# Performance work log

Measured on AMD Instinct MI355X. Metric: run time of the kernel, lower is better.

Reference implementation:

```python
import jax, jax.numpy as jnp
import numpy as np
import math

TILE_SIZE = 32
N_HEADS = 16
FACTOR = 5.0
MASK_VALUE = -1e9


def setup_inputs() -> dict:
    key = jax.random.key(0)
    ks = jax.random.split(key, 8)
    B, S, D = 2, 2048, 1024
    w = 0.02  # weight scale so attention logits stay in a sane range
    return {
        "query": jax.random.normal(ks[0], (B, S, D), jnp.float32),
        "key": jax.random.normal(ks[1], (B, S, D), jnp.float32),
        "value": jax.random.normal(ks[2], (B, S, D), jnp.float32),
        "mask": jnp.zeros((1, 1, S, S), jnp.float32),
        "Wq": jax.random.normal(ks[3], (D, D), jnp.float32) * w,
        "bq": jnp.zeros((D,), jnp.float32),
        "Wk": jax.random.normal(ks[4], (D, D), jnp.float32) * w,
        "bk": jnp.zeros((D,), jnp.float32),
        "Wv": jax.random.normal(ks[5], (D, D), jnp.float32) * w,
        "bv": jnp.zeros((D,), jnp.float32),
        "Wo": jax.random.normal(ks[6], (D, D), jnp.float32) * w,
        "bo": jnp.zeros((D,), jnp.float32),
        "q_valid_len": 2000,
        "k_valid_len": 1900,
    }


def _pad_to_multiple(x, multiple):
    L = x.shape[1]
    p = (-L) % multiple  # static
    if p:
        x = jnp.pad(x, ((0, 0), (0, p), (0, 0)))
    return x, L


def _split_heads(x, H):
    B, L, D = x.shape
    return x.reshape(B, L, H, D // H).transpose(0, 2, 1, 3)  # [B,H,L,hd]


def _forward(query, key, value, mask, Wq, bq, Wk, bk, Wv, bv, Wo, bo,
             q_valid_len, k_valid_len):
    B, Sq, D = query.shape
    H = N_HEADS
    hd = D // H
    q = query @ Wq.T + bq
    k = key @ Wk.T + bk
    v = value @ Wv.T + bv
    q, q_len_pad = _pad_to_multiple(q, TILE_SIZE)
    k, _ = _pad_to_multiple(k, TILE_SIZE)
    v, _ = _pad_to_multiple(v, TILE_SIZE)
    qh, kh, vh = _split_heads(q, H), _split_heads(k, H), _split_heads(v, H)
    Lq, Lk = qh.shape[2], kh.shape[2]

    # key padding mask [1,1,1,Lk]
    kpm = ((jnp.arange(Lk) >= k_valid_len).astype(jnp.float32) * MASK_VALUE)
    attn_mask = mask + kpm.reshape(1, 1, 1, Lk)

    # manual scaled-dot attention with bf16 cast of scores (stable softmax path)
    scores = jnp.einsum('bhqd,bhkd->bhqk', qh, kh) / math.sqrt(hd)
    scores = scores.astype(jnp.bfloat16) + attn_mask.astype(jnp.bfloat16)
    probs = jax.nn.softmax(scores, axis=-1).astype(vh.dtype)
    context = jnp.einsum('bhqk,bhkd->bhqd', probs, vh)

    # ProbSparse top-u query-selection mask (note: original passes q_len_pad,
    # the pre-padding length, as valid_length)
    u = max(1, int(FACTOR * math.log(max(2, q_valid_len))))
    q_norm = jnp.sum(qh * qh, axis=-1)  # [B,H,Lq]
    if q_len_pad < Lq:
        q_norm = jnp.where(jnp.arange(Lq) < q_len_pad, q_norm, MASK_VALUE)
    _, topk_idx = jax.lax.top_k(q_norm, u)  # [B,H,u]
    # scatter ones at top-u positions (indices unique -> one-hot sum == set)
    ps_mask = jnp.sum(jax.nn.one_hot(topk_idx, Lq, dtype=jnp.float32), axis=2)
    context = context * ps_mask[..., None]

    # merge heads, strip padding, output projection (dropout p=0 / eval)
    context = context.transpose(0, 2, 1, 3).reshape(B, Lq, D)[:, :Sq, :]
    return context @ Wo.T + bo


def reference(query, key, value, mask, Wq, bq, Wk, bk, Wv, bv, Wo, bo,
              q_valid_len, k_valid_len):
    return _forward(query, key, value, mask, Wq, bq, Wk, bk, Wv, bv, Wo, bo,
                    q_valid_len, k_valid_len)
```

## Files before the change

kernel.cpp:

```cpp
#include <hip/hip_runtime.h>

typedef unsigned short u16;
typedef __bf16 bf16x8 __attribute__((ext_vector_type(8)));
typedef float f32x4 __attribute__((ext_vector_type(4)));

__device__ __forceinline__ u16 f2bf(float f){
  unsigned int x = __float_as_uint(f);
  unsigned int r = (x + 0x7FFFu + ((x >> 16) & 1u)) >> 16;
  return (u16)r;
}
__device__ __forceinline__ float bf2f(u16 u){
  return __uint_as_float(((unsigned int)u) << 16);
}
__device__ __forceinline__ int compute_u(int qvlv){
  int mm = qvlv > 2 ? qvlv : 2;
  int u = (int)(5.0 * log((double)mm));
  if (u < 1) u = 1;
  if (u > 64) u = 64;
  return u;
}
__device__ __forceinline__ void gload_lds16(const void* g, void* l){
  __builtin_amdgcn_global_load_lds(
      (const __attribute__((address_space(1))) void*)g,
      (__attribute__((address_space(3))) void*)l, 16, 0, 0);
}

__global__ void expand_kernel(const float* __restrict__ xq, const float* __restrict__ xk,
                              const float* __restrict__ xv,
                              const float* __restrict__ wq, const float* __restrict__ wk,
                              const float* __restrict__ wv,
                              u16* __restrict__ X1, u16* __restrict__ X2,
                              u16* __restrict__ W1, u16* __restrict__ W2,
                              const float* __restrict__ Wo, float* __restrict__ WoT,
                              unsigned int* __restrict__ hmask)
{
  __shared__ float tile[32][33];
  int t = threadIdx.x;
  if (blockIdx.x >= 7680){
    int bid = blockIdx.x - 7680;
    int bx = (bid & 31) * 32, by = (bid >> 5) * 32;
    int tx = t & 31, ty = t >> 5;
#pragma unroll
    for (int r = 0; r < 4; ++r)
      tile[ty + r*8][tx] = Wo[(size_t)(by + ty + r*8) * 1024 + bx + tx];
    __syncthreads();
#pragma unroll
    for (int r = 0; r < 4; ++r)
      WoT[(size_t)(bx + ty + r*8) * 1024 + by + tx] = tile[tx][ty + r*8];
    return;
  }
  size_t g = (size_t)blockIdx.x * 256 + t;
  if (g < 4096) hmask[g] = 0;
  const float* src; u16 *d1, *d2;
  if (g < 1572864ull) {
    int p = (int)(g >> 19);
    size_t e = (g & 524287ull) * 8;
    src = (p == 0 ? xq : (p == 1 ? xk : xv)) + e;
    size_t o = (size_t)p * 4194304ull + e;
    d1 = X1 + o; d2 = X2 + o;
  } else {
    size_t wg = g - 1572864ull;
    int p = (int)(wg >> 17);
    size_t e = (wg & 131071ull) * 8;
    src = (p == 0 ? wq : (p == 1 ? wk : wv)) + e;
    size_t o = (size_t)p * 1048576ull + e;
    d1 = W1 + o; d2 = W2 + o;
  }
  float4 a = *reinterpret_cast<const float4*>(src);
  float4 b = *reinterpret_cast<const float4*>(src + 4);
  float xs[8] = {a.x, a.y, a.z, a.w, b.x, b.y, b.z, b.w};
  unsigned int hw[4], lw[4];
#pragma unroll
  for (int i = 0; i < 4; ++i){
    u16 h0 = f2bf(xs[2*i]);     u16 l0 = f2bf(xs[2*i]     - bf2f(h0));
    u16 h1 = f2bf(xs[2*i + 1]); u16 l1 = f2bf(xs[2*i + 1] - bf2f(h1));
    hw[i] = (unsigned int)h0 | ((unsigned int)h1 << 16);
    lw[i] = (unsigned int)l0 | ((unsigned int)l1 << 16);
  }
  *reinterpret_cast<uint4*>(d1) = make_uint4(hw[0], hw[1], hw[2], hw[3]);
  *reinterpret_cast<uint4*>(d2) = make_uint4(lw[0], lw[1], lw[2], lw[3]);
}

__global__ __launch_bounds__(512, 1) void gemm_proj(
    const u16* __restrict__ X1, const u16* __restrict__ X2,
    const u16* __restrict__ W1, const u16* __restrict__ W2,
    const float* __restrict__ bq, const float* __restrict__ bk, const float* __restrict__ bv,
    float* __restrict__ PROJ, float* __restrict__ qn)
{
  int z = blockIdx.z;
  int orig = blockIdx.x + blockIdx.y * 8;
  int wgid = (orig & 7) * 16 + (orig >> 3);
  int bx = wgid & 7, by = wgid >> 3;

  const u16* Xa0 = X1 + (size_t)z * 4194304;
  const u16* Xa1 = X2 + (size_t)z * 4194304;
  const u16* Wb0 = W1 + (size_t)z * 1048576;
  const u16* Wb1 = W2 + (size_t)z * 1048576;
  const float* bias = (z == 0) ? bq : (z == 1 ? bk : bv);
  float* C = PROJ + (size_t)z * 4194304;

  __shared__ __align__(16) u16 T[2 * 24576];
  u16* SET0 = T;
  u16* SET1 = T + 24576;

  int t = threadIdx.x;
  int wave = t >> 6, lane = t & 63;
  int wm = wave >> 1, wn = wave & 1;
  int lr = lane & 15, lk = lane >> 4;
  int rowA = by * 256, rowB = bx * 128;
  f32x4 acc[4][4] = {};
  bf16x8 afA[4], afB[4], bgA[4], bgB[4];

#define STAGEA(dstbase, G)                                                    \
  {                                                                           \
    _Pragma("unroll")                                                         \
    for (int i = 0; i < 2; ++i){                                              \
      int p = i * 512 + t;                                                    \
      int r = p >> 2;                                                         \
      int c = (p & 3) ^ ((r >> 1) & 3);                                       \
      gload_lds16(G + (size_t)(rowA + r) * 1024 + pk + c * 8,                 \
                  (dstbase) + p * 8);                                         \
    }                                                                         \
  }
#define STAGEB(dstbase, G)                                                    \
  {                                                                           \
    int p = t;                                                                \
    int r = p >> 2;                                                           \
    int c = (p & 3) ^ ((r >> 1) & 3);                                         \
    gload_lds16(G + (size_t)(rowB + r) * 1024 + pk + c * 8,                   \
                (dstbase) + p * 8);                                           \
  }
#define STAGE_SET(S)                                                          \
  {                                                                           \
    STAGEA((S), Xa0); STAGEA((S) + 8192, Xa1);                                \
    STAGEB((S) + 16384, Wb0); STAGEB((S) + 20480, Wb1);                       \
  }
#define LOADA(dst, tile)                                                      \
  {                                                                           \
    _Pragma("unroll")                                                         \
    for (int m = 0; m < 4; ++m){                                              \
      int r = wm * 64 + m * 16 + lr;                                          \
      dst[m] = *reinterpret_cast<const bf16x8*>(                              \
          &(tile)[r * 32 + ((lk ^ ((r >> 1) & 3)) << 3)]);                    \
    }                                                                         \
  }
#define LOADB(dst, tile)                                                      \
  {                                                                           \
    _Pragma("unroll")                                                         \
    for (int n = 0; n < 4; ++n){                                              \
      int r = wn * 64 + n * 16 + lr;                                          \
      dst[n] = *reinterpret_cast<const bf16x8*>(                              \
          &(tile)[r * 32 + ((lk ^ ((r >> 1) & 3)) << 3)]);                    \
    }                                                                         \
  }
#define GRPX(A_, B_)                                                          \
  {                                                                           \
    __builtin_amdgcn_s_setprio(1);                                            \
    _Pragma("unroll")                                                         \
    for (int m = 0; m < 4; ++m)                                               \
      _Pragma("unroll")                                                       \
      for (int n = 0; n < 4; ++n)                                             \
        acc[m][n] = __builtin_amdgcn_mfma_f32_16x16x32_bf16(A_[m], B_[n],     \
                                                            acc[m][n], 0,0,0);\
    __builtin_amdgcn_s_setprio(0);                                            \
  }

  {
    int pk = 0;
    STAGE_SET(SET0);
  }
  __syncthreads();

  for (int kt = 0; kt < 32; ++kt){
    u16* CUR = (kt & 1) ? SET1 : SET0;
    u16* NXT = (kt & 1) ? SET0 : SET1;
    if (kt < 31){
      int pk = (kt + 1) * 32;
      STAGE_SET(NXT);
    }
    __builtin_amdgcn_sched_barrier(0);
    u16* A0t = CUR;          u16* A1t = CUR + 8192;
    u16* B0t = CUR + 16384;  u16* B1t = CUR + 20480;
    LOADA(afA, A0t); LOADB(bgA, B0t);
    LOADB(bgB, B1t); GRPX(afA, bgA);
    LOADA(afB, A1t); GRPX(afA, bgB);
                     GRPX(afB, bgA);
    __syncthreads();
  }
#undef STAGEA
#undef STAGEB
#undef STAGE_SET
#undef LOADA
#undef LOADB
#undef GRPX

  if (z == 0){
    float sq[4][4] = {};
#pragma unroll
    for (int m = 0; m < 4; ++m){
      int row0 = by * 256 + wm * 64 + m * 16 + lk * 4;
#pragma unroll
      for (int n = 0; n < 4; ++n){
        int col = bx * 128 + wn * 64 + n * 16 + lr;
        float bb = bias[col];
#pragma unroll
        for (int j = 0; j < 4; ++j){
          float v = acc[m][n][j] + bb;
          C[(size_t)(row0 + j) * 1024 + col] = v;
          sq[m][j] += v * v;
        }
      }
    }
    int hh = bx * 2 + wn;
#pragma unroll
    for (int m = 0; m < 4; ++m){
#pragma unroll
      for (int j = 0; j < 4; ++j){
        float s = sq[m][j];
        s += __shfl_xor(s, 1);
        s += __shfl_xor(s, 2);
        s += __shfl_xor(s, 4);
        s += __shfl_xor(s, 8);
        if (lr == 0){
          int row = by * 256 + wm * 64 + m * 16 + lk * 4 + j;
          qn[(size_t)((row >> 11) * 16 + hh) * 2048 + (row & 2047)] = s;
        }
      }
    }
  } else if (z == 1){
    u16* KS = (u16*)C;
#pragma unroll
    for (int m = 0; m < 4; ++m){
      int r0 = by * 256 + wm * 64 + m * 16 + lk * 4;
      int b = r0 >> 11, kb = r0 & 2047;
#pragma unroll
      for (int n = 0; n < 4; ++n){
        int c = bx * 128 + wn * 64 + n * 16 + lr;
        float bb = bias[c];
        int h = c >> 6, d = c & 63;
#pragma unroll
        for (int j = 0; j < 4; ++j){
          float v = acc[m][n][j] + bb;
          u16 hi = f2bf(v);
          u16 lo = f2bf(v - bf2f(hi));
          size_t base = ((size_t)(b * 16 + h) * 2048 + (size_t)(kb + j)) * 128;
          KS[base + d] = hi;
          KS[base + 64 + d] = lo;
        }
      }
    }
  } else {
    u16* VT = (u16*)C;
#pragma unroll
    for (int m = 0; m < 4; ++m){
      int r0 = by * 256 + wm * 64 + m * 16 + lk * 4;
      int b = r0 >> 11, kb = r0 & 2047;
#pragma unroll
      for (int n = 0; n < 4; ++n){
        int c = bx * 128 + wn * 64 + n * 16 + lr;
        float bb = bias[c];
        int h = c >> 6, d = c & 63;
        u16 hi[4], lo[4];
#pragma unroll
        for (int j = 0; j < 4; ++j){
          float v = acc[m][n][j] + bb;
          hi[j] = f2bf(v);
          lo[j] = f2bf(v - bf2f(hi[j]));
        }
        size_t base = ((size_t)(b * 16 + h) * 128) * 2048 + (size_t)kb;
        *reinterpret_cast<ushort4*>(&VT[base + (size_t)d * 2048]) =
            make_ushort4(hi[0], hi[1], hi[2], hi[3]);
        *reinterpret_cast<ushort4*>(&VT[base + (size_t)(64 + d) * 2048]) =
            make_ushort4(lo[0], lo[1], lo[2], lo[3]);
      }
    }
  }
}

__global__ __launch_bounds__(256) void topk_kernel(
    const float* __restrict__ qn, int* __restrict__ topk,
    unsigned char* __restrict__ seli, unsigned int* __restrict__ hmask,
    const float* __restrict__ PROJ, u16* __restrict__ QS,
    const int* __restrict__ qvlp){
  int bh = blockIdx.x; int b = bh >> 4, h = bh & 15;
  int u = compute_u(qvlp[0]);
  int t = threadIdx.x;
  __shared__ int sidx_l[64];
  if (t < 64){
    int lane = t;
    float v[32];
#pragma unroll
    for (int j = 0; j < 32; ++j) v[j] = qn[(size_t)bh * 2048 + j * 64 + lane];
    for (int it = 0; it < u; ++it){
      float bv = v[0]; int bi = lane;
#pragma unroll
      for (int j = 1; j < 32; ++j){
        if (v[j] > bv){ bv = v[j]; bi = j * 64 + lane; }
      }
#pragma unroll
      for (int off = 1; off < 64; off <<= 1){
        float ov = __shfl_xor(bv, off);
        int   oi = __shfl_xor(bi, off);
        if (ov > bv || (ov == bv && oi < bi)){ bv = ov; bi = oi; }
      }
      if (lane == 0){
        topk[bh * 64 + it] = bi;
        seli[(size_t)bh * 2048 + bi] = (unsigned char)it;
        atomicOr(&hmask[b * 2048 + bi], 1u << h);
        sidx_l[it] = bi;
      }
#pragma unroll
      for (int j = 0; j < 32; ++j)
        if (j * 64 + lane == bi) v[j] = -3.4e38f;
    }
  }
  __syncthreads();
  for (int e = t; e < 64 * 64; e += 256){
    int i = e >> 6, d = e & 63;
    float v = 0.f;
    if (i < u) v = PROJ[(size_t)(b * 2048 + sidx_l[i]) * 1024 + h * 64 + d];
    u16 hi = f2bf(v);
    u16 lo = f2bf(v - bf2f(hi));
    QS[(size_t)bh * 8192 + i * 128 + d] = hi;
    QS[(size_t)bh * 8192 + i * 128 + 64 + d] = lo;
  }
}

__global__ __launch_bounds__(256) void scores_mfma(
    const u16* __restrict__ QS, const u16* __restrict__ KS,
    const int* __restrict__ topk, const float* __restrict__ maskp,
    u16* __restrict__ sc, const int* __restrict__ qvlp, const int* __restrict__ kvlp)
{
  int bh = blockIdx.y;
  int kvlv = kvlp[0]; if (kvlv > 2048) kvlv = 2048; if (kvlv < 0) kvlv = 0;
  int u = compute_u(qvlp[0]);
  int k0 = blockIdx.x * 128;
  if (k0 >= kvlv) return;
  int t = threadIdx.x, wave = t >> 6, lane = t & 63;
  int lr = lane & 15, lk = lane >> 4;
  __shared__ int idx_l[64];
  if (t < 64) idx_l[t] = (t < u) ? topk[bh * 64 + t] : 0;
  __syncthreads();
  const u16* Qb = QS + (size_t)bh * 8192;
  const u16* Kb = KS + (size_t)bh * 2048 * 128;
  bf16x8 ah[2], al[2];
#pragma unroll
  for (int ks = 0; ks < 2; ++ks){
    const u16* qrow = &Qb[(wave * 16 + lr) * 128];
    ah[ks] = *reinterpret_cast<const bf16x8*>(&qrow[ks * 32 + lk * 8]);
    al[ks] = *reinterpret_cast<const bf16x8*>(&qrow[64 + ks * 32 + lk * 8]);
  }
  f32x4 acc[8] = {};
#pragma unroll
  for (int n = 0; n < 8; ++n){
    const u16* krow = &Kb[(size_t)(k0 + n * 16 + lr) * 128];
    bf16x8 bh0 = *reinterpret_cast<const bf16x8*>(&krow[lk * 8]);
    bf16x8 bh1 = *reinterpret_cast<const bf16x8*>(&krow[32 + lk * 8]);
    bf16x8 bl0 = *reinterpret_cast<const bf16x8*>(&krow[64 + lk * 8]);
    bf16x8 bl1 = *reinterpret_cast<const bf16x8*>(&krow[96 + lk * 8]);
    acc[n] = __builtin_amdgcn_mfma_f32_16x16x32_bf16(ah[0], bh0, acc[n], 0, 0, 0);
    acc[n] = __builtin_amdgcn_mfma_f32_16x16x32_bf16(ah[0], bl0, acc[n], 0, 0, 0);
    acc[n] = __builtin_amdgcn_mfma_f32_16x16x32_bf16(al[0], bh0, acc[n], 0, 0, 0);
    acc[n] = __builtin_amdgcn_mfma_f32_16x16x32_bf16(al[0], bl0, acc[n], 0, 0, 0);
    acc[n] = __builtin_amdgcn_mfma_f32_16x16x32_bf16(ah[1], bh1, acc[n], 0, 0, 0);
    acc[n] = __builtin_amdgcn_mfma_f32_16x16x32_bf16(ah[1], bl1, acc[n], 0, 0, 0);
    acc[n] = __builtin_amdgcn_mfma_f32_16x16x32_bf16(al[1], bh1, acc[n], 0, 0, 0);
    acc[n] = __builtin_amdgcn_mfma_f32_16x16x32_bf16(al[1], bl1, acc[n], 0, 0, 0);
  }
#pragma unroll
  for (int n = 0; n < 8; ++n){
    int k = k0 + n * 16 + lr;
    if (k >= kvlv) continue;
#pragma unroll
    for (int j = 0; j < 4; ++j){
      int i = wave * 16 + lk * 4 + j;
      if (i >= u) continue;
      float s = acc[n][j] * 0.125f;
      u16 xb = f2bf(s);
      u16 mb = f2bf(maskp[(size_t)idx_l[i] * 2048 + k]);
      u16 xm = f2bf(bf2f(xb) + bf2f(mb));
      sc[(size_t)(bh * 64 + i) * 2048 + k] = xm;
    }
  }
}

__global__ void softmax_kernel(u16* __restrict__ sc, const int* __restrict__ qvlp,
                               const int* __restrict__ kvlp){
  int bh = blockIdx.y, i = blockIdx.x;
  int u = compute_u(qvlp[0]);
  if (i >= u) return;
  int kvlv = kvlp[0]; if (kvlv > 2048) kvlv = 2048; if (kvlv < 0) kvlv = 0;
  u16* row = sc + (size_t)(bh * 64 + i) * 2048;
  int t = threadIdx.x;
  float x[8];
  float lm = -3.4e38f;
#pragma unroll
  for (int j = 0; j < 8; ++j){
    int k = t + j * 256;
    x[j] = (k < kvlv) ? bf2f(row[k]) : -3.4e38f;
    lm = fmaxf(lm, x[j]);
  }
  __shared__ float red[256];
  red[t] = lm; __syncthreads();
  for (int s = 128; s > 0; s >>= 1){ if (t < s) red[t] = fmaxf(red[t], red[t+s]); __syncthreads(); }
  float m = red[0];
  __syncthreads();
  float e[8]; float ls = 0.f;
#pragma unroll
  for (int j = 0; j < 8; ++j){
    int k = t + j * 256;
    if (k < kvlv){
      u16 ub = f2bf(x[j] - m);
      u16 eb = f2bf(expf(bf2f(ub)));
      e[j] = bf2f(eb);
      ls += e[j];
    } else e[j] = 0.f;
  }
  red[t] = ls; __syncthreads();
  for (int s = 128; s > 0; s >>= 1){ if (t < s) red[t] += red[t+s]; __syncthreads(); }
  float S = red[0];
  float Sb = bf2f(f2bf(S));
#pragma unroll
  for (int j = 0; j < 8; ++j){
    int k = t + j * 256;
    if (k < 2048) row[k] = (k < kvlv) ? f2bf(e[j] / Sb) : (u16)0;
  }
}

__global__ void pv_mfma(const u16* __restrict__ probs, const u16* __restrict__ VT,
                        float* __restrict__ part, const int* __restrict__ kvlp)
{
  int bh = blockIdx.y; int b = bh >> 4, h = bh & 15;
  int kvlv = kvlp[0]; if (kvlv > 2048) kvlv = 2048; if (kvlv < 0) kvlv = 0;
  int kc = blockIdx.x;
  int k0 = kc * 128;
  if (k0 >= kvlv) return;
  int t = threadIdx.x, w = t >> 6, lane = t & 63;
  int lr = lane & 15, lk = lane >> 4;
  const u16* Pb = probs + (size_t)bh * 64 * 2048;
  const u16* Vb = VT + (size_t)(b * 16 + h) * 128 * 2048;
  f32x4 acc[4] = {};
#pragma unroll
  for (int ks = 0; ks < 4; ++ks){
    int kk = k0 + ks * 32 + lk * 8;
    bf16x8 A0 = *reinterpret_cast<const bf16x8*>(Pb + (size_t)(lr     ) * 2048 + kk);
    bf16x8 A1 = *reinterpret_cast<const bf16x8*>(Pb + (size_t)(lr + 16) * 2048 + kk);
    bf16x8 A2 = *reinterpret_cast<const bf16x8*>(Pb + (size_t)(lr + 32) * 2048 + kk);
    bf16x8 A3 = *reinterpret_cast<const bf16x8*>(Pb + (size_t)(lr + 48) * 2048 + kk);
    bf16x8 Bh = *reinterpret_cast<const bf16x8*>(Vb + (size_t)(w * 16 + lr     ) * 2048 + kk);
    bf16x8 Bl = *reinterpret_cast<const bf16x8*>(Vb + (size_t)(w * 16 + lr + 64) * 2048 + kk);
    acc[0] = __builtin_amdgcn_mfma_f32_16x16x32_bf16(A0, Bh, acc[0], 0, 0, 0);
    acc[1] = __builtin_amdgcn_mfma_f32_16x16x32_bf16(A1, Bh, acc[1], 0, 0, 0);
    acc[2] = __builtin_amdgcn_mfma_f32_16x16x32_bf16(A2, Bh, acc[2], 0, 0, 0);
    acc[3] = __builtin_amdgcn_mfma_f32_16x16x32_bf16(A3, Bh, acc[3], 0, 0, 0);
    acc[0] = __builtin_amdgcn_mfma_f32_16x16x32_bf16(A0, Bl, acc[0], 0, 0, 0);
    acc[1] = __builtin_amdgcn_mfma_f32_16x16x32_bf16(A1, Bl, acc[1], 0, 0, 0);
    acc[2] = __builtin_amdgcn_mfma_f32_16x16x32_bf16(A2, Bl, acc[2], 0, 0, 0);
    acc[3] = __builtin_amdgcn_mfma_f32_16x16x32_bf16(A3, Bl, acc[3], 0, 0, 0);
  }
  float* pc = part + (size_t)(kc * 32 + bh) * 64 * 64;
#pragma unroll
  for (int m = 0; m < 4; ++m){
    int row = m * 16 + lk * 4;
#pragma unroll
    for (int j = 0; j < 4; ++j)
      pc[(size_t)(row + j) * 64 + w * 16 + lr] = acc[m][j];
  }
}

__global__ void outproj_kernel(const float* __restrict__ part, const float* __restrict__ WoT,
                               const float* __restrict__ bo, const unsigned int* __restrict__ hmask,
                               const unsigned char* __restrict__ seli, float* __restrict__ out,
                               const int* __restrict__ kvlp){
  int row = blockIdx.x;
  int b = row >> 11, l = row & 2047;
  int t = threadIdx.x;
  int kvlv = kvlp[0]; if (kvlv > 2048) kvlv = 2048; if (kvlv < 0) kvlv = 0;
  int kcmax = (kvlv + 127) / 128;
  float acc[4];
#pragma unroll
  for (int r = 0; r < 4; ++r) acc[r] = bo[t + r * 256];
  unsigned int m = hmask[row];
  __shared__ float clds[64];
  while (m){
    int h = __ffs(m) - 1; m &= (m - 1);
    int bh = b * 16 + h;
    int i = (int)seli[(size_t)bh * 2048 + l];
    __syncthreads();
    if (t < 64){
      float s = 0.f;
      for (int kc = 0; kc < kcmax; ++kc)
        s += part[(size_t)((kc * 32 + bh) * 64 + i) * 64 + t];
      clds[t] = s;
    }
    __syncthreads();
    for (int j = 0; j < 64; ++j){
      float c = clds[j];
      const float* wrow = &WoT[(size_t)(h * 64 + j) * 1024];
#pragma unroll
      for (int r = 0; r < 4; ++r) acc[r] += c * wrow[t + r * 256];
    }
  }
  float* orow = out + (size_t)row * 1024;
#pragma unroll
  for (int r = 0; r < 4; ++r) orow[t + r * 256] = acc[r];
}

__global__ void fail_fill(float* o, int n){
  int i = blockIdx.x * 256 + threadIdx.x;
  if (i < n) o[i] = 12345.0f;
}

extern "C" void kernel_launch(void* const* d_in, const int* in_sizes, int n_in,
                              void* d_out, int out_size, void* d_ws, size_t ws_size,
                              hipStream_t stream)
{
  const float* query = (const float*)d_in[0];
  const float* key   = (const float*)d_in[1];
  const float* value = (const float*)d_in[2];
  const float* maskp = (const float*)d_in[3];
  const float* Wq = (const float*)d_in[4];
  const float* bq = (const float*)d_in[5];
  const float* Wk = (const float*)d_in[6];
  const float* bk = (const float*)d_in[7];
  const float* Wv = (const float*)d_in[8];
  const float* bv = (const float*)d_in[9];
  const float* Wo = (const float*)d_in[10];
  const float* bo = (const float*)d_in[11];
  const int* qvl = (const int*)d_in[12];
  const int* kvl = (const int*)d_in[13];
  float* out = (float*)d_out;

  char* ws = (char*)d_ws;
  size_t off = 0;
  auto alloc = [&](size_t bytes) -> void* {
    void* p = ws + off;
    off = (off + bytes + 255) & ~(size_t)255;
    return p;
  };
  u16* X1 = (u16*)alloc(3ull * 4194304 * 2);
  u16* X2 = (u16*)alloc(3ull * 4194304 * 2);
  u16* W1 = (u16*)alloc(3ull * 1048576 * 2);
  u16* W2 = (u16*)alloc(3ull * 1048576 * 2);
  float* PROJ = (float*)alloc(3ull * 4194304 * 4);
  float* WOT  = (float*)alloc(4194304ull);
  float* QN   = (float*)alloc(2ull * 16 * 2048 * 4);
  int*   TOPK = (int*)alloc(2ull * 16 * 64 * 4);
  unsigned char* SELI = (unsigned char*)alloc(2ull * 16 * 2048);
  unsigned int* HMASK = (unsigned int*)alloc(2ull * 2048 * 4);
  u16*   SC   = (u16*)alloc(2048ull * 2048 * 2);
  u16*   QS   = (u16*)alloc(32ull * 64 * 128 * 2);

  u16* KS = (u16*)(PROJ + 1ull * 4194304);
  u16* VT = (u16*)(PROJ + 2ull * 4194304);
  float* PART = (float*)X1;

  if (ws_size < off){
    fail_fill<<<(out_size + 255) / 256, 256, 0, stream>>>(out, out_size);
    return;
  }

  expand_kernel<<<8704, 256, 0, stream>>>(query, key, value, Wq, Wk, Wv,
                                          X1, X2, W1, W2, Wo, WOT, HMASK);
  gemm_proj<<<dim3(8, 16, 3), 512, 0, stream>>>(X1, X2, W1, W2, bq, bk, bv, PROJ, QN);
  topk_kernel<<<32, 256, 0, stream>>>(QN, TOPK, SELI, HMASK, PROJ, QS, qvl);
  scores_mfma<<<dim3(16, 32), 256, 0, stream>>>(QS, KS, TOPK, maskp, SC, qvl, kvl);
  softmax_kernel<<<dim3(64, 32), 256, 0, stream>>>(SC, qvl, kvl);
  pv_mfma<<<dim3(16, 32), 256, 0, stream>>>(SC, VT, PART, kvl);
  outproj_kernel<<<4096, 256, 0, stream>>>(PART, WOT, bo, HMASK, SELI, out, kvl);
}
```

Baseline: 252.1 us.

## Load projection weight fragments directly from global into registers, skipping LDS

The B-operand (weight) tiles of the fused QKV projection GEMM are now read straight from global memory into register fragments, double-buffered in registers one k-step ahead, instead of being staged through LDS. This shrinks the LDS footprint and removes LDS reads for B. The loop is unrolled by two to alternate register buffers. The cost is extra VGPR pressure, and the global B loads are uncoalesced and repeated by the waves that share the same columns.

New measurement: 323.9 us. 1.28x slower.

```diff
diff --git a/kernel.cpp b/kernel.cpp
--- a/kernel.cpp
+++ b/kernel.cpp
@@ -99,9 +99,9 @@
   const float* bias = (z == 0) ? bq : (z == 1 ? bk : bv);
   float* C = PROJ + (size_t)z * 4194304;
 
-  __shared__ __align__(16) u16 T[2 * 24576];
+  __shared__ __align__(16) u16 T[2 * 16384];
   u16* SET0 = T;
-  u16* SET1 = T + 24576;
+  u16* SET1 = T + 16384;
 
   int t = threadIdx.x;
   int wave = t >> 6, lane = t & 63;
@@ -109,7 +109,8 @@
   int lr = lane & 15, lk = lane >> 4;
   int rowA = by * 256, rowB = bx * 128;
   f32x4 acc[4][4] = {};
-  bf16x8 afA[4], afB[4], bgA[4], bgB[4];
+  bf16x8 afA[4], afB[4];
+  bf16x8 bgP0[4], bgP1[4], bgQ0[4], bgQ1[4];
 
 #define STAGEA(dstbase, G)                                                    \
   {                                                                           \
@@ -122,18 +123,14 @@
                   (dstbase) + p * 8);                                         \
     }                                                                         \
   }
-#define STAGEB(dstbase, G)                                                    \
+#define LOADBG(dst, G, PK)                                                    \
   {                                                                           \
-    int p = t;                                                                \
-    int r = p >> 2;                                                           \
-    int c = (p & 3) ^ ((r >> 1) & 3);                                         \
-    gload_lds16(G + (size_t)(rowB + r) * 1024 + pk + c * 8,                   \
-                (dstbase) + p * 8);                                           \
-  }
-#define STAGE_SET(S)                                                          \
-  {                                                                           \
-    STAGEA((S), Xa0); STAGEA((S) + 8192, Xa1);                                \
-    STAGEB((S) + 16384, Wb0); STAGEB((S) + 20480, Wb1);                       \
+    _Pragma("unroll")                                                         \
+    for (int n = 0; n < 4; ++n){                                              \
+      int r = rowB + wn * 64 + n * 16 + lr;                                   \
+      dst[n] = *reinterpret_cast<const bf16x8*>(                              \
+          G + (size_t)r * 1024 + (PK) + lk * 8);                              \
+    }                                                                         \
   }
 #define LOADA(dst, tile)                                                      \
   {                                                                           \
@@ -141,15 +138,6 @@
     for (int m = 0; m < 4; ++m){                                              \
       int r = wm * 64 + m * 16 + lr;                                          \
       dst[m] = *reinterpret_cast<const bf16x8*>(                              \
-          &(tile)[r * 32 + ((lk ^ ((r >> 1) & 3)) << 3)]);                    \
-    }                                                                         \
-  }
-#define LOADB(dst, tile)                                                      \
-  {                                                                           \
-    _Pragma("unroll")                                                         \
-    for (int n = 0; n < 4; ++n){                                              \
-      int r = wn * 64 + n * 16 + lr;                                          \
-      dst[n] = *reinterpret_cast<const bf16x8*>(                              \
           &(tile)[r * 32 + ((lk ^ ((r >> 1) & 3)) << 3)]);                    \
     }                                                                         \
   }
@@ -164,35 +152,41 @@
                                                             acc[m][n], 0,0,0);\
     __builtin_amdgcn_s_setprio(0);                                            \
   }
+#define CHUNK(KT, PAR, CB0, CB1, NB0, NB1)                                    \
+  {                                                                           \
+    u16* CUR = (PAR) ? SET1 : SET0;                                           \
+    u16* NXT = (PAR) ? SET0 : SET1;                                           \
+    if ((KT) < 31){                                                           \
+      int pk = ((KT) + 1) * 32;                                               \
+      STAGEA(NXT, Xa0); STAGEA(NXT + 8192, Xa1);                              \
+      LOADBG(NB0, Wb0, pk);                                                   \
+      LOADBG(NB1, Wb1, pk);                                                   \
+    }                                                                         \
+    __builtin_amdgcn_sched_barrier(0);                                        \
+    u16* A0t = CUR;  u16* A1t = CUR + 8192;                                   \
+    LOADA(afA, A0t); GRPX(afA, CB0);                               \
+    LOADA(afB, A1t); GRPX(afA, CB1);                               \
+                     GRPX(afB, CB0);                               \
+    __syncthreads();                       \
+  }
 
   {
     int pk = 0;
-    STAGE_SET(SET0);
+    STAGEA(SET0, Xa0); STAGEA(SET0 + 8192, Xa1);
+    LOADBG(bgP0, Wb0, 0);
+    LOADBG(bgP1, Wb1, 0);
   }
   __syncthreads();
 
-  for (int kt = 0; kt < 32; ++kt){
-    u16* CUR = (kt & 1) ? SET1 : SET0;
-    u16* NXT = (kt & 1) ? SET0 : SET1;
-    if (kt < 31){
-      int pk = (kt + 1) * 32;
-      STAGE_SET(NXT);
-    }
-    __builtin_amdgcn_sched_barrier(0);
-    u16* A0t = CUR;          u16* A1t = CUR + 8192;
-    u16* B0t = CUR + 16384;  u16* B1t = CUR + 20480;
-    LOADA(afA, A0t); LOADB(bgA, B0t);
-    LOADB(bgB, B1t); GRPX(afA, bgA);
-    LOADA(afB, A1t); GRPX(afA, bgB);
-                     GRPX(afB, bgA);
-    __syncthreads();
+  for (int kt = 0; kt < 32; kt += 2){
+    CHUNK(kt,     0, bgP0, bgP1, bgQ0, bgQ1);
+    CHUNK(kt + 1, 1, bgQ0, bgQ1, bgP0, bgP1);
   }
 #undef STAGEA
-#undef STAGEB
-#undef STAGE_SET
+#undef LOADBG
 #undef LOADA
-#undef LOADB
 #undef GRPX
+#undef CHUNK
 
   if (z == 0){
     float sq[4][4] = {};
```
